# Optimization experiments

Measured on AMD Instinct MI355X. Metric: run time of the kernel, lower is better.

## Reference

```python
import math
import jax, jax.numpy as jnp
import numpy as np

B, C, N, K = 16, 64, 2048, 20

def setup_inputs() -> dict:
    key = jax.random.key(0)
    x = jax.random.normal(key, (B, C, N), dtype=jnp.float32)
    local_idx = jnp.zeros((B, N), dtype=bool)  # unused in dgcnn variant
    return {"x": x, "k": K, "local_idx": local_idx}

def _gather_points(points, idx):
    # points: (B, N, C), idx: (B, N, k) -> (B, N, k, C)
    return jax.vmap(lambda p, i: p[i])(points, idx)

def reference(x, k, local_idx):
    b, c, n = x.shape
    xt = jnp.swapaxes(x, 1, 2)  # (B, N, C)
    # negative squared pairwise distance: -||xi||^2 + 2 xi.xj - ||xj||^2
    inner = 2.0 * jnp.einsum('bnc,bmc->bnm', xt, xt)
    xx = jnp.sum(xt * xt, axis=-1)  # (B, N)
    pd = -xx[:, :, None] + inner - xx[:, None, :]
    _, idx = jax.lax.top_k(pd, k)  # (B, N, k) nearest neighbors
    knn_x = _gather_points(xt, idx)  # (B, N, k, C)
    # per-channel topk over the k neighbors, then mean
    k2 = math.ceil(k * 2 / 3)
    vals = jax.lax.top_k(jnp.swapaxes(knn_x, 2, 3), k2)[0]  # (B, N, C, k2)
    x1 = jnp.mean(vals, axis=-1)  # (B, N, C)
    # gather smoothed features at neighbor indices
    feat = _gather_points(x1, idx)  # (B, N, k, C)
    x_exp = jnp.broadcast_to(xt[:, :, None, :], (b, n, k, c))
    feature = jnp.concatenate([feat - x_exp, x_exp], axis=-1)  # (B, N, k, 2C)
    feature = jnp.transpose(feature, (0, 3, 1, 2))  # (B, 2C, N, k)
    idx_flat = (idx + jnp.arange(b, dtype=idx.dtype)[:, None, None] * n).reshape(-1)
    return feature, idx_flat
```

## Files before the change

### kernel.cpp

```cpp
#include <hip/hip_runtime.h>
#include <cstdint>
#include <cstddef>
#include <math.h>

#define BB 16
#define CC 64
#define NN 2048
#define KK 20
#define K2 14
#define TQ 8
#define NC 26

typedef float nfloat4 __attribute__((ext_vector_type(4)));

__global__ __launch_bounds__(256) void prep_kernel(const float* __restrict__ x,
                                                   float* __restrict__ xt,
                                                   float* __restrict__ xxf,
                                                   double* __restrict__ xxd) {
    __shared__ float s_t[64][65];
    int b = blockIdx.x >> 5;
    int n0 = (blockIdx.x & 31) * 64;
    const float* xb = x + (size_t)b * CC * NN;
    int tid = threadIdx.x;
    int cq = tid >> 6;
    int nl = tid & 63;

#pragma unroll
    for (int r = 0; r < 16; ++r) {
        int c = r * 4 + cq;
        s_t[c][nl] = xb[c * NN + n0 + nl];
    }
    __syncthreads();

#pragma unroll
    for (int r = 0; r < 16; ++r) {
        int n = r * 4 + cq;
        xt[((size_t)b * NN + n0 + n) * CC + nl] = s_t[nl][n];
    }

    if (tid < 64) {
        double s = 0.0;
#pragma unroll
        for (int c = 0; c < CC; ++c) {
            double v = (double)s_t[c][tid];
            s += v * v;
        }
        xxd[b * NN + n0 + tid] = s;
        xxf[b * NN + n0 + tid] = (float)s;
    }
}

__global__ __launch_bounds__(512) void knn_kernel(const float* __restrict__ x,
                                                  const float* __restrict__ xt,
                                                  const float* __restrict__ xxf,
                                                  const double* __restrict__ xxd,
                                                  int* __restrict__ idx_ws,
                                                  float* __restrict__ idx_out) {
    __shared__ float s_pd[TQ][NN];
    __shared__ __align__(16) float s_q[CC][TQ];
    __shared__ float s_sv[TQ][64];
    __shared__ int   s_si[TQ][64];

    int tid = threadIdx.x;
    int b = blockIdx.x >> 8;
    int n0 = (blockIdx.x & 255) * TQ;
    const float* xb = x + (size_t)b * CC * NN;

    { int c = tid >> 3, qq = tid & 7; s_q[c][qq] = xb[c * NN + n0 + qq]; }
    __syncthreads();

    {
        float4 xa = *(const float4*)(xxf + b * NN + n0);
        float4 xc = *(const float4*)(xxf + b * NN + n0 + 4);
        float xxn[TQ] = {xa.x, xa.y, xa.z, xa.w, xc.x, xc.y, xc.z, xc.w};

        int m = tid * 4;
        float acc[TQ][4];
#pragma unroll
        for (int q = 0; q < TQ; ++q)
#pragma unroll
            for (int i = 0; i < 4; ++i) acc[q][i] = 0.f;

        for (int c = 0; c < CC; ++c) {
            float4 xv = *(const float4*)(xb + c * NN + m);
            float4 qa = *(const float4*)(&s_q[c][0]);
            float4 qb = *(const float4*)(&s_q[c][4]);
            float xs[4] = {xv.x, xv.y, xv.z, xv.w};
            float qs[TQ] = {qa.x, qa.y, qa.z, qa.w, qb.x, qb.y, qb.z, qb.w};
#pragma unroll
            for (int q = 0; q < TQ; ++q)
#pragma unroll
                for (int i = 0; i < 4; ++i) acc[q][i] += qs[q] * xs[i];
        }
        float4 xm4 = *(const float4*)(xxf + b * NN + m);
        float xms[4] = {xm4.x, xm4.y, xm4.z, xm4.w};
#pragma unroll
        for (int q = 0; q < TQ; ++q) {
            float4 pdv;
            pdv.x = (2.f * acc[q][0] - xxn[q]) - xms[0];
            pdv.y = (2.f * acc[q][1] - xxn[q]) - xms[1];
            pdv.z = (2.f * acc[q][2] - xxn[q]) - xms[2];
            pdv.w = (2.f * acc[q][3] - xxn[q]) - xms[3];
            *(float4*)(&s_pd[q][m]) = pdv;
        }
    }
    __syncthreads();

    int q = tid >> 6;
    int lane = tid & 63;
    const float* pd = s_pd[q];

    float v[32];
#pragma unroll
    for (int r = 0; r < 32; ++r) v[r] = pd[lane + (r << 6)];

    float lmax = v[0]; int lr = 0;
#pragma unroll
    for (int r = 1; r < 32; ++r)
        if (v[r] > lmax) { lmax = v[r]; lr = r; }

    float sv = lmax;
#pragma unroll
    for (int k = 2; k <= 64; k <<= 1) {
#pragma unroll
        for (int j = k >> 1; j > 0; j >>= 1) {
            float o = __shfl_xor(sv, j);
            bool dird = ((lane & k) == 0);
            bool first = ((lane & j) == 0);
            sv = (first == dird) ? fmaxf(sv, o) : fminf(sv, o);
        }
    }
    float tau = __shfl(sv, 25);

    int cnt = 0;
#pragma unroll
    for (int r = 0; r < 32; ++r) cnt += (v[r] >= tau) ? 1 : 0;
    int incl = cnt;
#pragma unroll
    for (int off = 1; off < 64; off <<= 1) {
        int o = __shfl_up(incl, off);
        if (lane >= off) incl += o;
    }
    int S = __shfl(incl, 63);

    float fv = -INFINITY;
    int fi = 0x7fffffff;
    if (S <= 64) {
        int w = incl - cnt;
#pragma unroll
        for (int r = 0; r < 32; ++r) {
            if (v[r] >= tau) { s_sv[q][w] = v[r]; s_si[q][w] = lane + (r << 6); ++w; }
        }
        if (lane < S) { fv = s_sv[q][lane]; fi = s_si[q][lane]; }
    } else {
        for (int t = 0; t < NC; ++t) {
            float bv = lmax; int bi = lane + (lr << 6);
#pragma unroll
            for (int off = 32; off; off >>= 1) {
                float ov = __shfl_xor(bv, off);
                int oi = __shfl_xor(bi, off);
                if (ov > bv || (ov == bv && oi < bi)) { bv = ov; bi = oi; }
            }
            if (lane == t) { fv = bv; fi = bi; }
            if ((bi & 63) == lane) {
                int rsel = bi >> 6;
#pragma unroll
                for (int r = 0; r < 32; ++r) if (r == rsel) v[r] = -INFINITY;
                lmax = v[0]; lr = 0;
#pragma unroll
                for (int r = 1; r < 32; ++r)
                    if (v[r] > lmax) { lmax = v[r]; lr = r; }
            }
        }
    }

#pragma unroll
    for (int k = 2; k <= 64; k <<= 1) {
#pragma unroll
        for (int j = k >> 1; j > 0; j >>= 1) {
            float ov = __shfl_xor(fv, j);
            int oi = __shfl_xor(fi, j);
            bool dird = ((lane & k) == 0);
            bool first = ((lane & j) == 0);
            bool better = (fv > ov) || (fv == ov && fi < oi);
            if (better != (first == dird)) { fv = ov; fi = oi; }
        }
    }

    float* s_c = (float*)&s_pd[q][0];
    const float* xtb = xt + (size_t)b * NN * CC;
    int nq = n0 + q;

#pragma unroll
    for (int t = 0; t < NC; ++t) {
        int cand = __shfl(fi, t);
        s_c[lane * 27 + t] = xtb[(size_t)cand * CC + lane];
    }

    double accd = 0.0;
    for (int c = 0; c < CC; ++c) {
        double qc = (double)s_q[c][q];
        double cd = (double)s_c[c * 27 + lane];
        accd = fma(qc, cd, accd);
    }

    double val = -INFINITY;
    int idxq = 0x7fffffff;
    if (lane < NC) {
        val = 2.0 * accd - xxd[b * NN + nq] - xxd[b * NN + fi];
        idxq = fi;
    }

#pragma unroll
    for (int k = 2; k <= 32; k <<= 1) {
#pragma unroll
        for (int j = k >> 1; j > 0; j >>= 1) {
            double ov = __shfl_xor(val, j, 32);
            int oi = __shfl_xor(idxq, j, 32);
            bool dird = ((lane & k) == 0);
            bool first = ((lane & j) == 0);
            bool better = (val > ov) || (val == ov && idxq < oi);
            if (better != (first == dird)) { val = ov; idxq = oi; }
        }
    }

    if (lane < KK) {
        size_t obase = ((size_t)b * NN + nq) * KK;
        idx_ws[obase + lane] = idxq;
        idx_out[obase + lane] = (float)(idxq + b * NN);
    }
}

__global__ __launch_bounds__(256) void x1_kernel(const float* __restrict__ xt,
                                                 const int* __restrict__ idx_ws,
                                                 float* __restrict__ x1t) {
    __shared__ int s_idx[16][KK];
    __shared__ float s_out[64][17];
    int tid = threadIdx.x;
    int b = blockIdx.x >> 7;
    int n0 = (blockIdx.x & 127) * 16;
    const float* xtb = xt + (size_t)b * NN * CC;

    for (int i = tid; i < 16 * KK; i += 256)
        s_idx[i / KK][i % KK] = idx_ws[((size_t)b * NN + n0) * KK + i];
    __syncthreads();

    int pl = tid >> 6, c = tid & 63;
#pragma unroll
    for (int it = 0; it < 4; ++it) {
        int nl = it * 4 + pl;
        float vals[KK];
        float sum = 0.f;
#pragma unroll
        for (int j = 0; j < KK; ++j) {
            vals[j] = xtb[(size_t)s_idx[nl][j] * CC + c];
            sum += vals[j];
        }
#pragma unroll
        for (int t = 0; t < KK - K2; ++t) {
            float worst = INFINITY;
            int wj = 0;
#pragma unroll
            for (int j = 0; j < KK; ++j)
                if (vals[j] < worst) { worst = vals[j]; wj = j; }
            sum -= worst;
            vals[wj] = INFINITY;
        }
        s_out[c][nl] = sum / (float)K2;
    }
    __syncthreads();

    int cw = tid >> 2, nw = (tid & 3) * 4;
    float4 v = make_float4(s_out[cw][nw], s_out[cw][nw + 1],
                           s_out[cw][nw + 2], s_out[cw][nw + 3]);
    *(float4*)(&x1t[((size_t)b * CC + cw) * NN + n0 + nw]) = v;
}

__global__ __launch_bounds__(256) void feat_kernel(const float* __restrict__ x,
                                                   const float* __restrict__ x1t,
                                                   const int* __restrict__ idx_ws,
                                                   float* __restrict__ out) {
    int bc = blockIdx.x;
    int b = bc >> 7, ch = bc & 127;
    const float* xb = x + (size_t)b * CC * NN;
    float* o = out + (size_t)bc * NN * KK;
    const int* idxb = idx_ws + (size_t)b * NN * KK;

    if (ch < CC) {
        const float* row = x1t + ((size_t)b * CC + ch) * NN;
        const float* xr = xb + ch * NN;
        for (int it = 0; it < 40; ++it) {
            unsigned e = (it * 256 + threadIdx.x) * 4;
            int4 id4 = *(const int4*)(idxb + e);
            nfloat4 o4;
            o4.x = row[id4.x] - xr[(e    ) / KK];
            o4.y = row[id4.y] - xr[(e + 1) / KK];
            o4.z = row[id4.z] - xr[(e + 2) / KK];
            o4.w = row[id4.w] - xr[(e + 3) / KK];
            __builtin_nontemporal_store(o4, (nfloat4*)(o + e));
        }
    } else {
        const float* xr = xb + (ch - CC) * NN;
        for (int it = 0; it < 40; ++it) {
            unsigned e = (it * 256 + threadIdx.x) * 4;
            nfloat4 o4;
            o4.x = xr[(e    ) / KK];
            o4.y = xr[(e + 1) / KK];
            o4.z = xr[(e + 2) / KK];
            o4.w = xr[(e + 3) / KK];
            __builtin_nontemporal_store(o4, (nfloat4*)(o + e));
        }
    }
}

extern "C" void kernel_launch(void* const* d_in, const int* in_sizes, int n_in,
                              void* d_out, int out_size, void* d_ws, size_t ws_size,
                              hipStream_t stream) {
    const float* x = (const float*)d_in[0];
    float* out = (float*)d_out;

    char* ws = (char*)d_ws;
    float* xt   = (float*)ws;
    float* x1t  = (float*)(ws + (size_t)8388608);
    double* xxd = (double*)(ws + (size_t)16777216);
    float* xxf  = (float*)(ws + (size_t)17039360);
    int* idx_ws = (int*)(ws + (size_t)17170432);

    float* idx_out = out + (size_t)BB * 2 * CC * NN * KK;

    prep_kernel<<<BB * (NN / 64), 256, 0, stream>>>(x, xt, xxf, xxd);
    knn_kernel<<<BB * (NN / TQ), 512, 0, stream>>>(x, xt, xxf, xxd, idx_ws, idx_out);
    x1_kernel<<<BB * (NN / 16), 256, 0, stream>>>(xt, idx_ws, x1t);
    feat_kernel<<<BB * 2 * CC, 256, 0, stream>>>(x, x1t, idx_ws, out);
}
```

Before: 602.7 us.

## Compute kNN distances with split-bf16 MFMA and 16 queries per block

Replaces the FP32 scalar FMA Gram computation in the kNN kernel with bf16 MFMA instructions. FP32 accuracy is approximated by splitting each value into high and low bf16 parts and summing three cross products. Prep now also writes bf16 hi/lo copies of the transposed points, using the output buffer as scratch before feat_kernel overwrites it. Blocks grow to 1024 threads and 16 queries, with padded shared rows and a shared norm cache. The cost is extra prep traffic and large shared memory that may limit occupancy, plus possible tie or precision changes in the top-k selection.

```diff
diff --git a/kernel.cpp b/kernel.cpp
--- a/kernel.cpp
+++ b/kernel.cpp
@@ -8,13 +8,24 @@
 #define NN 2048
 #define KK 20
 #define K2 14
-#define TQ 8
+#define QB 16
 #define NC 26
+#define SP 2064
 
 typedef float nfloat4 __attribute__((ext_vector_type(4)));
+typedef __attribute__((ext_vector_type(8))) short bf16x8;
+typedef __attribute__((ext_vector_type(4))) float f32x4;
+typedef unsigned short u16;
+
+static __device__ __forceinline__ u16 f2bf(float f) {
+    unsigned u = __float_as_uint(f);
+    return (u16)((u + 0x7fffu + ((u >> 16) & 1u)) >> 16);
+}
 
 __global__ __launch_bounds__(256) void prep_kernel(const float* __restrict__ x,
                                                    float* __restrict__ xt,
+                                                   u16* __restrict__ xth,
+                                                   u16* __restrict__ xtl,
                                                    float* __restrict__ xxf,
                                                    double* __restrict__ xxd) {
     __shared__ float s_t[64][65];
@@ -35,7 +46,14 @@
 #pragma unroll
     for (int r = 0; r < 16; ++r) {
         int n = r * 4 + cq;
-        xt[((size_t)b * NN + n0 + n) * CC + nl] = s_t[nl][n];
+        float f = s_t[nl][n];
+        size_t o = ((size_t)b * NN + n0 + n) * CC + nl;
+        xt[o] = f;
+        u16 h = f2bf(f);
+        float hf = __uint_as_float((unsigned)h << 16);
+        u16 l = f2bf(f - hf);
+        xth[o] = h;
+        xtl[o] = l;
     }
 
     if (tid < 64) {
@@ -50,65 +68,83 @@
     }
 }
 
-__global__ __launch_bounds__(512) void knn_kernel(const float* __restrict__ x,
-                                                  const float* __restrict__ xt,
-                                                  const float* __restrict__ xxf,
-                                                  const double* __restrict__ xxd,
-                                                  int* __restrict__ idx_ws,
-                                                  float* __restrict__ idx_out) {
-    __shared__ float s_pd[TQ][NN];
-    __shared__ __align__(16) float s_q[CC][TQ];
-    __shared__ float s_sv[TQ][64];
-    __shared__ int   s_si[TQ][64];
+__global__ __launch_bounds__(1024, 2) void knn_kernel(const float* __restrict__ x,
+                                                      const float* __restrict__ xt,
+                                                      const u16* __restrict__ xth,
+                                                      const u16* __restrict__ xtl,
+                                                      const float* __restrict__ xxf,
+                                                      const double* __restrict__ xxd,
+                                                      int* __restrict__ idx_ws,
+                                                      float* __restrict__ idx_out) {
+    __shared__ float s_pd[QB][SP];
+    __shared__ float s_xx[NN];
+    __shared__ __align__(16) float s_q[CC][QB];
+    __shared__ float s_sv[QB][64];
+    __shared__ int   s_si[QB][64];
 
     int tid = threadIdx.x;
-    int b = blockIdx.x >> 8;
-    int n0 = (blockIdx.x & 255) * TQ;
+    int b = blockIdx.x >> 7;
+    int n0 = (blockIdx.x & 127) * QB;
     const float* xb = x + (size_t)b * CC * NN;
 
-    { int c = tid >> 3, qq = tid & 7; s_q[c][qq] = xb[c * NN + n0 + qq]; }
-    __syncthreads();
+    { int c = tid >> 4, qq = tid & 15; s_q[c][qq] = xb[c * NN + n0 + qq]; }
+    s_xx[tid] = xxf[b * NN + tid];
+    s_xx[tid + 1024] = xxf[b * NN + 1024 + tid];
+    __syncthreads();
+
+    int w = tid >> 6;
+    int lane = tid & 63;
+    int ar = lane & 15, ag = lane >> 4;
 
     {
-        float4 xa = *(const float4*)(xxf + b * NN + n0);
-        float4 xc = *(const float4*)(xxf + b * NN + n0 + 4);
-        float xxn[TQ] = {xa.x, xa.y, xa.z, xa.w, xc.x, xc.y, xc.z, xc.w};
-
-        int m = tid * 4;
-        float acc[TQ][4];
-#pragma unroll
-        for (int q = 0; q < TQ; ++q)
-#pragma unroll
-            for (int i = 0; i < 4; ++i) acc[q][i] = 0.f;
-
-        for (int c = 0; c < CC; ++c) {
-            float4 xv = *(const float4*)(xb + c * NN + m);
-            float4 qa = *(const float4*)(&s_q[c][0]);
-            float4 qb = *(const float4*)(&s_q[c][4]);
-            float xs[4] = {xv.x, xv.y, xv.z, xv.w};
-            float qs[TQ] = {qa.x, qa.y, qa.z, qa.w, qb.x, qb.y, qb.z, qb.w};
-#pragma unroll
-            for (int q = 0; q < TQ; ++q)
-#pragma unroll
-                for (int i = 0; i < 4; ++i) acc[q][i] += qs[q] * xs[i];
-        }
-        float4 xm4 = *(const float4*)(xxf + b * NN + m);
-        float xms[4] = {xm4.x, xm4.y, xm4.z, xm4.w};
-#pragma unroll
-        for (int q = 0; q < TQ; ++q) {
-            float4 pdv;
-            pdv.x = (2.f * acc[q][0] - xxn[q]) - xms[0];
-            pdv.y = (2.f * acc[q][1] - xxn[q]) - xms[1];
-            pdv.z = (2.f * acc[q][2] - xxn[q]) - xms[2];
-            pdv.w = (2.f * acc[q][3] - xxn[q]) - xms[3];
-            *(float4*)(&s_pd[q][m]) = pdv;
-        }
-    }
-    __syncthreads();
-
-    int q = tid >> 6;
-    int lane = tid & 63;
-    const float* pd = s_pd[q];
+        const u16* xhb = xth + (size_t)b * NN * CC;
+        const u16* xlb = xtl + (size_t)b * NN * CC;
+        const u16* aph = xhb + (size_t)(n0 + ar) * CC + ag * 8;
+        const u16* apl = xlb + (size_t)(n0 + ar) * CC + ag * 8;
+        bf16x8 ah0 = *(const bf16x8*)(aph);
+        bf16x8 ah1 = *(const bf16x8*)(aph + 32);
+        bf16x8 al0 = *(const bf16x8*)(apl);
+        bf16x8 al1 = *(const bf16x8*)(apl + 32);
+
+        int p0 = w * 128;
+        f32x4 acc[8];
+#pragma unroll
+        for (int t = 0; t < 8; ++t)
+#pragma unroll
+            for (int i = 0; i < 4; ++i) acc[t][i] = 0.f;
+
+#pragma unroll
+        for (int t = 0; t < 8; ++t) {
+            const u16* bph = xhb + (size_t)(p0 + t * 16 + ar) * CC + ag * 8;
+            const u16* bpl = xlb + (size_t)(p0 + t * 16 + ar) * CC + ag * 8;
+            bf16x8 bh0 = *(const bf16x8*)(bph);
+            bf16x8 bh1 = *(const bf16x8*)(bph + 32);
+            bf16x8 bl0 = *(const bf16x8*)(bpl);
+            bf16x8 bl1 = *(const bf16x8*)(bpl + 32);
+            acc[t] = __builtin_amdgcn_mfma_f32_16x16x32_bf16(ah0, bh0, acc[t], 0, 0, 0);
+            acc[t] = __builtin_amdgcn_mfma_f32_16x16x32_bf16(al0, bh0, acc[t], 0, 0, 0);
+            acc[t] = __builtin_amdgcn_mfma_f32_16x16x32_bf16(ah0, bl0, acc[t], 0, 0, 0);
+            acc[t] = __builtin_amdgcn_mfma_f32_16x16x32_bf16(ah1, bh1, acc[t], 0, 0, 0);
+            acc[t] = __builtin_amdgcn_mfma_f32_16x16x32_bf16(al1, bh1, acc[t], 0, 0, 0);
+            acc[t] = __builtin_amdgcn_mfma_f32_16x16x32_bf16(ah1, bl1, acc[t], 0, 0, 0);
+        }
+
+        float qn[4];
+#pragma unroll
+        for (int r = 0; r < 4; ++r) qn[r] = s_xx[n0 + ag * 4 + r];
+#pragma unroll
+        for (int t = 0; t < 8; ++t) {
+            int p = p0 + t * 16 + ar;
+            float xxp = s_xx[p];
+#pragma unroll
+            for (int r = 0; r < 4; ++r)
+                s_pd[ag * 4 + r][p] = (2.f * acc[t][r] - qn[r]) - xxp;
+        }
+    }
+    __syncthreads();
+
+    int q = w;
+    const float* pd = &s_pd[q][0];
 
     float v[32];
 #pragma unroll
@@ -146,10 +182,10 @@
     float fv = -INFINITY;
     int fi = 0x7fffffff;
     if (S <= 64) {
-        int w = incl - cnt;
+        int wr = incl - cnt;
 #pragma unroll
         for (int r = 0; r < 32; ++r) {
-            if (v[r] >= tau) { s_sv[q][w] = v[r]; s_si[q][w] = lane + (r << 6); ++w; }
+            if (v[r] >= tau) { s_sv[q][wr] = v[r]; s_si[q][wr] = lane + (r << 6); ++wr; }
         }
         if (lane < S) { fv = s_sv[q][lane]; fi = s_si[q][lane]; }
     } else {
@@ -326,10 +362,13 @@
     float* xxf  = (float*)(ws + (size_t)17039360);
     int* idx_ws = (int*)(ws + (size_t)17170432);
 
+    u16* xth = (u16*)out;
+    u16* xtl = (u16*)((char*)out + (size_t)8388608);
+
     float* idx_out = out + (size_t)BB * 2 * CC * NN * KK;
 
-    prep_kernel<<<BB * (NN / 64), 256, 0, stream>>>(x, xt, xxf, xxd);
-    knn_kernel<<<BB * (NN / TQ), 512, 0, stream>>>(x, xt, xxf, xxd, idx_ws, idx_out);
+    prep_kernel<<<BB * (NN / 64), 256, 0, stream>>>(x, xt, xth, xtl, xxf, xxd);
+    knn_kernel<<<BB * (NN / QB), 1024, 0, stream>>>(x, xt, xth, xtl, xxf, xxd, idx_ws, idx_out);
     x1_kernel<<<BB * (NN / 16), 256, 0, stream>>>(xt, idx_ws, x1t);
     feat_kernel<<<BB * 2 * CC, 256, 0, stream>>>(x, x1t, idx_ws, out);
 }
```

Result: slower. 658.6 us (+9.3%).

## Store pairwise distances as half in LDS and vectorize candidate refinement

Applied to the files above, without the earlier changes.

The distance tile in shared memory is stored as fp16 instead of fp32, which halves LDS use and targets higher occupancy, now requested as 6 blocks per CU through launch bounds. The candidate rescoring step no longer stages candidate rows in LDS; each lane reads its candidate row directly from global memory with float4 loads and a transposed query copy, and accumulates in double with four partial sums. The fp16 rounding could alter the coarse candidate selection near ties, and correctness then rests on the 26-candidate double-precision refinement.

```diff
diff --git a/kernel.cpp b/kernel.cpp
--- a/kernel.cpp
+++ b/kernel.cpp
@@ -1,4 +1,5 @@
 #include <hip/hip_runtime.h>
+#include <hip/hip_fp16.h>
 #include <cstdint>
 #include <cstddef>
 #include <math.h>
@@ -10,6 +11,7 @@
 #define K2 14
 #define TQ 8
 #define NC 26
+#define SPH 2052
 
 typedef float nfloat4 __attribute__((ext_vector_type(4)));
 
@@ -50,14 +52,15 @@
     }
 }
 
-__global__ __launch_bounds__(512) void knn_kernel(const float* __restrict__ x,
-                                                  const float* __restrict__ xt,
-                                                  const float* __restrict__ xxf,
-                                                  const double* __restrict__ xxd,
-                                                  int* __restrict__ idx_ws,
-                                                  float* __restrict__ idx_out) {
-    __shared__ float s_pd[TQ][NN];
+__global__ __launch_bounds__(512, 6) void knn_kernel(const float* __restrict__ x,
+                                                     const float* __restrict__ xt,
+                                                     const float* __restrict__ xxf,
+                                                     const double* __restrict__ xxd,
+                                                     int* __restrict__ idx_ws,
+                                                     float* __restrict__ idx_out) {
+    __shared__ __half s_pd[TQ][SPH];
     __shared__ __align__(16) float s_q[CC][TQ];
+    __shared__ __align__(16) float s_qT[TQ][CC];
     __shared__ float s_sv[TQ][64];
     __shared__ int   s_si[TQ][64];
 
@@ -66,7 +69,12 @@
     int n0 = (blockIdx.x & 255) * TQ;
     const float* xb = x + (size_t)b * CC * NN;
 
-    { int c = tid >> 3, qq = tid & 7; s_q[c][qq] = xb[c * NN + n0 + qq]; }
+    {
+        int c = tid >> 3, qq = tid & 7;
+        float qv = xb[c * NN + n0 + qq];
+        s_q[c][qq] = qv;
+        s_qT[qq][c] = qv;
+    }
     __syncthreads();
 
     {
@@ -101,18 +109,21 @@
             pdv.y = (2.f * acc[q][1] - xxn[q]) - xms[1];
             pdv.z = (2.f * acc[q][2] - xxn[q]) - xms[2];
             pdv.w = (2.f * acc[q][3] - xxn[q]) - xms[3];
-            *(float4*)(&s_pd[q][m]) = pdv;
+            __half2 h01 = __floats2half2_rn(pdv.x, pdv.y);
+            __half2 h23 = __floats2half2_rn(pdv.z, pdv.w);
+            *(__half2*)(&s_pd[q][m]) = h01;
+            *(__half2*)(&s_pd[q][m + 2]) = h23;
         }
     }
     __syncthreads();
 
     int q = tid >> 6;
     int lane = tid & 63;
-    const float* pd = s_pd[q];
+    const __half* pd = &s_pd[q][0];
 
     float v[32];
 #pragma unroll
-    for (int r = 0; r < 32; ++r) v[r] = pd[lane + (r << 6)];
+    for (int r = 0; r < 32; ++r) v[r] = __half2float(pd[lane + (r << 6)]);
 
     float lmax = v[0]; int lr = 0;
 #pragma unroll
@@ -187,21 +198,22 @@
         }
     }
 
-    float* s_c = (float*)&s_pd[q][0];
-    const float* xtb = xt + (size_t)b * NN * CC;
     int nq = n0 + q;
-
-#pragma unroll
-    for (int t = 0; t < NC; ++t) {
-        int cand = __shfl(fi, t);
-        s_c[lane * 27 + t] = xtb[(size_t)cand * CC + lane];
-    }
-
     double accd = 0.0;
-    for (int c = 0; c < CC; ++c) {
-        double qc = (double)s_q[c][q];
-        double cd = (double)s_c[c * 27 + lane];
-        accd = fma(qc, cd, accd);
+    if (lane < NC) {
+        const float* crow = xt + (size_t)b * NN * CC + (size_t)fi * CC;
+        const float* qrow = &s_qT[q][0];
+        double a0 = 0.0, a1 = 0.0, a2 = 0.0, a3 = 0.0;
+#pragma unroll
+        for (int j = 0; j < 16; ++j) {
+            float4 cv = *(const float4*)(crow + j * 4);
+            float4 qv = *(const float4*)(qrow + j * 4);
+            a0 = fma((double)qv.x, (double)cv.x, a0);
+            a1 = fma((double)qv.y, (double)cv.y, a1);
+            a2 = fma((double)qv.z, (double)cv.z, a2);
+            a3 = fma((double)qv.w, (double)cv.w, a3);
+        }
+        accd = (a0 + a1) + (a2 + a3);
     }
 
     double val = -INFINITY;
```

After: 593.7 us. No clear change (-1.5%).
